# Kernel tuning notes

Measured on AMD Instinct MI355X. Metric: run time of the kernel, lower is better.

Reference implementation:

```python
import jax, jax.numpy as jnp
import numpy as np

NUM_HEADS = 8
C = 512


def setup_inputs() -> dict:
    key = jax.random.key(0)
    ks = jax.random.split(key, 8)
    B, D, H, W = 1, 16, 16, 16
    x = jax.random.normal(ks[0], (B, C, D, H, W), dtype=jnp.float32)
    s = 1.0 / np.sqrt(C)
    Wq = jax.random.normal(ks[1], (C, C), dtype=jnp.float32) * s
    Wk = jax.random.normal(ks[2], (C, C), dtype=jnp.float32) * s
    Wv = jax.random.normal(ks[3], (C, C), dtype=jnp.float32) * s
    bq = jax.random.normal(ks[4], (C,), dtype=jnp.float32) * 0.01
    bk = jax.random.normal(ks[5], (C,), dtype=jnp.float32) * 0.01
    bv = jax.random.normal(ks[6], (C,), dtype=jnp.float32) * 0.01
    # torch inits gamma to 0; use 0.5 so the attention branch contributes
    gamma = jnp.full((1,), 0.5, dtype=jnp.float32)
    return {"x": x, "Wq": Wq, "bq": bq, "Wk": Wk, "bk": bk, "Wv": Wv, "bv": bv, "gamma": gamma}


def _attn(x, Wq, bq, Wk, bk, Wv, bv, gamma):
    B, Cc, D, H, W = x.shape
    nh = NUM_HEADS
    hd = Cc // nh
    N = D * H * W

    def proj(Wm, bm):
        # 1x1x1 Conv3d == channel GEMM
        y = jnp.einsum('oc,bcdhw->bodhw', Wm, x) + bm[None, :, None, None, None]
        y = y.reshape(B, nh, hd, D, H, W)            # [B, nh, hd, D, H, W]
        y = jnp.moveaxis(y, 2, -1)                    # [B, nh, D, H, W, hd]
        return y.reshape(B * nh, N, hd)               # [B*nh, N, hd]

    q = proj(Wq, bq)
    k = proj(Wk, bk)
    v = proj(Wv, bv)

    # NOTE: original module has NO 1/sqrt(head_dim) scaling -- faithful.
    energy = jnp.einsum('bnd,bmd->bnm', q, k)         # [B*nh, N, N]
    attention = jax.nn.softmax(energy, axis=-1)
    out = jnp.einsum('bnm,bmd->bnd', attention, v)    # [B*nh, N, hd]

    # Faithful (buggy-in-original) reshape: [B, N, nh, hd] row-major into [B, C, D, H, W]
    out = out.reshape(B, nh, N, hd).transpose(0, 2, 1, 3).reshape(B, Cc, D, H, W)
    return gamma[0] * out + x


def reference(x, Wq, bq, Wk, bk, Wv, bv, gamma):
    return _attn(x, Wq, bq, Wk, bk, Wv, bv, gamma)
```

## Files before the change

### kernel.cpp

```cpp
#include <hip/hip_runtime.h>

typedef unsigned short u16;
typedef __attribute__((ext_vector_type(4))) float f32x4;
typedef __attribute__((ext_vector_type(8))) short s16x8;
typedef __attribute__((ext_vector_type(4))) unsigned short u16x4;
typedef __attribute__((ext_vector_type(8))) unsigned short u16x8;
typedef __attribute__((ext_vector_type(2))) unsigned int u32x2;

#define MFMA(a, b, c) __builtin_amdgcn_mfma_f32_16x16x32_bf16((a), (b), (c), 0, 0, 0)

#define XT_HI 0u
#define XT_LO 2097152u
#define W_HI  4194304u
#define W_LO  4980736u
#define Q_HI  5767168u
#define Q_LO  7864320u
#define K_HI  9961472u
#define K_LO  12058624u
#define V_HI  14155776u
#define V_LO  16252928u
#define WS_BYTES_U16 36700160u

__device__ __forceinline__ u16 f2bf(float f) {
  union { float f; unsigned u; } v; v.f = f;
  unsigned r = v.u + 0x7fffu + ((v.u >> 16) & 1u);
  return (u16)(r >> 16);
}
__device__ __forceinline__ float bf2f(u16 h) {
  union { unsigned u; float f; } v; v.u = ((unsigned)h) << 16;
  return v.f;
}
__device__ __forceinline__ unsigned pk2(float a, float b) {
  return (unsigned)f2bf(a) | ((unsigned)f2bf(b) << 16);
}
__device__ __forceinline__ void gload16(const void* g, void* l) {
  __builtin_amdgcn_global_load_lds(
      (const __attribute__((address_space(1))) void*)g,
      (__attribute__((address_space(3))) void*)l, 16, 0, 0);
}

__global__ __launch_bounds__(256) void prep_w(const float* __restrict__ wq,
                                              const float* __restrict__ wk,
                                              const float* __restrict__ wv,
                                              u16* __restrict__ ws) {
  unsigned t = blockIdx.x * 256u + threadIdx.x;
  unsigned idx = t * 4u;
  unsigned which = idx >> 18;
  unsigned rem = idx & 262143u;
  const float* src = (which == 0) ? wq : (which == 1) ? wk : wv;
  f32x4 v = *(const f32x4*)(src + rem);
  u16x4 h, l;
#pragma unroll
  for (int i = 0; i < 4; ++i) {
    u16 hb = f2bf(v[i]);
    h[i] = hb;
    l[i] = f2bf(v[i] - bf2f(hb));
  }
  *(u16x4*)(ws + W_HI + idx) = h;
  *(u16x4*)(ws + W_LO + idx) = l;
}

__global__ __launch_bounds__(256) void prep_xt(const float* __restrict__ x,
                                               u16* __restrict__ ws) {
  __shared__ float tile[64][65];
  unsigned t = threadIdx.x;
  unsigned n0 = blockIdx.x * 64u, c0 = blockIdx.y * 64u;
  unsigned cl = t >> 2, ns = (t & 3u) * 16u;
  const float* src = x + (c0 + cl) * 4096u + n0 + ns;
#pragma unroll
  for (int j = 0; j < 16; j += 4) {
    f32x4 v = *(const f32x4*)(src + j);
#pragma unroll
    for (int e = 0; e < 4; ++e) tile[cl][ns + j + e] = v[e];
  }
  __syncthreads();
  unsigned nl = t >> 2, cs = (t & 3u) * 16u;
  u16x8 vh0, vh1, vl0, vl1;
#pragma unroll
  for (int j = 0; j < 16; ++j) {
    float v = tile[cs + j][nl];
    u16 hb = f2bf(v);
    u16 lb = f2bf(v - bf2f(hb));
    if (j < 8) { vh0[j] = hb; vl0[j] = lb; }
    else       { vh1[j - 8] = hb; vl1[j - 8] = lb; }
  }
  unsigned off = (n0 + nl) * 512u + c0 + cs;
  *(u16x8*)(ws + XT_HI + off) = vh0;
  *(u16x8*)(ws + XT_HI + off + 8u) = vh1;
  *(u16x8*)(ws + XT_LO + off) = vl0;
  *(u16x8*)(ws + XT_LO + off + 8u) = vl1;
}

__global__ __launch_bounds__(256) void proj(const float* __restrict__ bq,
                                            const float* __restrict__ bk,
                                            const float* __restrict__ bv,
                                            u16* __restrict__ ws) {
  __shared__ u16 sm[24576];
  const unsigned t = threadIdx.x, w = t >> 6, lane = t & 63u;
  const unsigned g4 = lane >> 4, c = lane & 15u;
  const unsigned z = blockIdx.z;
  const unsigned m0 = blockIdx.y * 64u, n0 = blockIdx.x * 128u;
  const unsigned wo = w >> 1, wn = w & 1u;

  const u16* WHp = ws + W_HI + z * 262144u;
  const u16* WLp = ws + W_LO + z * 262144u;
  const u16* XH = ws + XT_HI;
  const u16* XL = ws + XT_LO;

  f32x4 acc[2][4];
#pragma unroll
  for (int a = 0; a < 2; ++a)
#pragma unroll
    for (int b = 0; b < 4; ++b) acc[a][b] = (f32x4){0.f, 0.f, 0.f, 0.f};

  const unsigned r_l = lane >> 3;
  const unsigned cl_ = lane & 7u;

  for (unsigned it = 0; it < 8; ++it) {
    unsigned k0 = it * 64u;
#pragma unroll
    for (unsigned j = 0; j < 12; ++j) {
      unsigned s = w * 12u + j;
      if (s < 8u) {
        unsigned r = 8u * s + r_l; unsigned cg = cl_ ^ (r & 7u);
        gload16(WHp + (m0 + r) * 512u + k0 + 8u * cg, sm + s * 512u);
      } else if (s < 16u) {
        unsigned sl = s - 8u; unsigned r = 8u * sl + r_l; unsigned cg = cl_ ^ (r & 7u);
        gload16(WLp + (m0 + r) * 512u + k0 + 8u * cg, sm + 4096u + sl * 512u);
      } else if (s < 32u) {
        unsigned sl = s - 16u; unsigned r = 8u * sl + r_l; unsigned cg = cl_ ^ (r & 7u);
        gload16(XH + (n0 + r) * 512u + k0 + 8u * cg, sm + 8192u + sl * 512u);
      } else {
        unsigned sl = s - 32u; unsigned r = 8u * sl + r_l; unsigned cg = cl_ ^ (r & 7u);
        gload16(XL + (n0 + r) * 512u + k0 + 8u * cg, sm + 16384u + sl * 512u);
      }
    }
    __syncthreads();

    s16x8 ah[2][2], al[2][2];
#pragma unroll
    for (int mr = 0; mr < 2; ++mr)
#pragma unroll
      for (int ks = 0; ks < 2; ++ks) {
        unsigned row = 32u * wo + 16u * mr + c;
        unsigned idx = row * 64u + (((g4 + 4u * ks) ^ (row & 7u)) * 8u);
        ah[mr][ks] = *(const s16x8*)(sm + idx);
        al[mr][ks] = *(const s16x8*)(sm + 4096u + idx);
      }
#pragma unroll
    for (int ks = 0; ks < 2; ++ks)
#pragma unroll
      for (int nr = 0; nr < 4; ++nr) {
        unsigned row = 64u * wn + 16u * nr + c;
        unsigned idx = row * 64u + (((g4 + 4u * ks) ^ (row & 7u)) * 8u);
        s16x8 bh = *(const s16x8*)(sm + 8192u + idx);
        s16x8 bl = *(const s16x8*)(sm + 16384u + idx);
#pragma unroll
        for (int mr = 0; mr < 2; ++mr) {
          acc[mr][nr] = MFMA(ah[mr][ks], bh, acc[mr][nr]);
          acc[mr][nr] = MFMA(ah[mr][ks], bl, acc[mr][nr]);
          acc[mr][nr] = MFMA(al[mr][ks], bh, acc[mr][nr]);
        }
      }
    __syncthreads();
  }

  const float* bias = (z == 0) ? bq : (z == 1) ? bk : bv;
  const unsigned obase = m0 + 32u * wo;
#pragma unroll
  for (int mr = 0; mr < 2; ++mr) {
    f32x4 b4 = *(const f32x4*)(bias + obase + 16u * mr + 4u * g4);
#pragma unroll
    for (int nr = 0; nr < 4; ++nr) {
      unsigned n = n0 + 64u * wn + 16u * nr + c;
      float v4[4];
#pragma unroll
      for (int i = 0; i < 4; ++i) v4[i] = acc[mr][nr][i] + b4[i];
      if (z < 2u) {
        unsigned d0 = 32u * wo + 16u * mr + 4u * g4;
        unsigned off = (blockIdx.y * 4096u + n) * 64u + d0;
        u16* dh = ws + (z ? K_HI : Q_HI) + off;
        u16* dl = ws + (z ? K_LO : Q_LO) + off;
        u16x4 h4, l4;
#pragma unroll
        for (int i = 0; i < 4; ++i) {
          u16 hb = f2bf(v4[i]);
          h4[i] = hb;
          l4[i] = f2bf(v4[i] - bf2f(hb));
        }
        *(u16x4*)dh = h4;
        *(u16x4*)dl = l4;
      } else {
#pragma unroll
        for (int i = 0; i < 4; ++i) {
          unsigned o = obase + 16u * mr + 4u * g4 + i;
          ws[V_HI + o * 4096u + n] = f2bf(v4[i]);
        }
      }
    }
  }
}

__global__ __launch_bounds__(256) void attn(const u16* __restrict__ ws,
                                            float* __restrict__ ows,
                                            float* __restrict__ lws) {
  extern __shared__ u16 sm[];
  const unsigned t = threadIdx.x, w = t >> 6, lane = t & 63u;
  const unsigned g4 = lane >> 4, c = lane & 15u;
  const unsigned h = blockIdx.y, sp = blockIdx.z;
  const unsigned q0 = blockIdx.x * 128u;

  const u16* QHp = ws + Q_HI; const u16* QLp = ws + Q_LO;
  const u16* KHp = ws + K_HI; const u16* KLp = ws + K_LO;
  const u16* VHp = ws + V_HI;

  s16x8 qh[2][2], ql[2][2];
#pragma unroll
  for (int mq = 0; mq < 2; ++mq)
#pragma unroll
    for (int ks = 0; ks < 2; ++ks) {
      unsigned q = q0 + 32u * w + 16u * mq + c;
      unsigned off = (h * 4096u + q) * 64u + 8u * g4 + 32u * ks;
      qh[mq][ks] = *(const s16x8*)(QHp + off);
      ql[mq][ks] = *(const s16x8*)(QLp + off);
    }

  f32x4 O[2][4];
#pragma unroll
  for (int a = 0; a < 2; ++a)
#pragma unroll
    for (int b = 0; b < 4; ++b) O[a][b] = (f32x4){0.f, 0.f, 0.f, 0.f};
  float lr[2] = {0.f, 0.f};

  const unsigned r_l = lane >> 3, cl_ = lane & 7u;
  u16* Pw = sm + 24576u + w * 2048u;

  auto stage = [&](unsigned b, unsigned ch) {
    unsigned n0 = sp * 2048u + ch * 64u;
#pragma unroll
    for (unsigned j = 0; j < 6u; ++j) {
      unsigned s = w * 6u + j;
      unsigned pl = s >> 3, sl = s & 7u;
      unsigned r = 8u * sl + r_l;
      unsigned cg = cl_ ^ (r & 7u);
      const u16* gsrc;
      if (pl == 0u)      gsrc = KHp + (h * 4096u + n0 + r) * 64u + 8u * cg;
      else if (pl == 1u) gsrc = KLp + (h * 4096u + n0 + r) * 64u + 8u * cg;
      else               gsrc = VHp + (h * 64u + r) * 4096u + n0 + 8u * cg;
      gload16(gsrc, sm + b * 12288u + pl * 4096u + sl * 512u);
    }
  };

  stage(0u, 0u);
  __syncthreads();

  unsigned cur = 0u;
  for (unsigned ch = 0; ch < 32u; ++ch) {
    if (ch < 31u) stage(cur ^ 1u, ch + 1u);
    const unsigned kb = cur * 12288u;

    f32x4 S[2][4];
#pragma unroll
    for (int a = 0; a < 2; ++a)
#pragma unroll
      for (int b = 0; b < 4; ++b) S[a][b] = (f32x4){0.f, 0.f, 0.f, 0.f};
#pragma unroll
    for (int ks = 0; ks < 2; ++ks)
#pragma unroll
      for (int nr = 0; nr < 4; ++nr) {
        unsigned row = 16u * nr + c;
        unsigned idx = kb + row * 64u + (((g4 + 4u * ks) ^ (row & 7u)) * 8u);
        s16x8 kh = *(const s16x8*)(sm + idx);
        s16x8 kl = *(const s16x8*)(sm + 4096u + idx);
#pragma unroll
        for (int mq = 0; mq < 2; ++mq) {
          S[mq][nr] = MFMA(kh, qh[mq][ks], S[mq][nr]);
          S[mq][nr] = MFMA(kl, qh[mq][ks], S[mq][nr]);
          S[mq][nr] = MFMA(kh, ql[mq][ks], S[mq][nr]);
        }
      }

#pragma unroll
    for (int mq = 0; mq < 2; ++mq) {
      unsigned q = 16u * mq + c;
      float ls = 0.f;
#pragma unroll
      for (int nr = 0; nr < 4; ++nr) {
        f32x4 s = S[mq][nr];
        float p0 = __expf(s[0] - 40.0f);
        float p1 = __expf(s[1] - 40.0f);
        float p2 = __expf(s[2] - 40.0f);
        float p3 = __expf(s[3] - 40.0f);
        ls += (p0 + p1) + (p2 + p3);
        u32x2 pv;
        pv[0] = pk2(p0, p1);
        pv[1] = pk2(p2, p3);
        unsigned off = q * 64u + (((2u * nr + (g4 >> 1)) ^ (c & 7u)) * 8u) + (g4 & 1u) * 4u;
        *(u32x2*)(Pw + off) = pv;
      }
      ls += __shfl_xor(ls, 16);
      ls += __shfl_xor(ls, 32);
      lr[mq] += ls;
    }

#pragma unroll
    for (int ks = 0; ks < 2; ++ks) {
      s16x8 pa[2];
#pragma unroll
      for (int mr = 0; mr < 2; ++mr)
        pa[mr] = *(const s16x8*)(Pw + (16u * mr + c) * 64u +
                                 (((g4 + 4u * ks) ^ (c & 7u)) * 8u));
#pragma unroll
      for (int nr = 0; nr < 4; ++nr) {
        unsigned row = 16u * nr + c;
        unsigned idx = kb + 8192u + row * 64u + (((g4 + 4u * ks) ^ (row & 7u)) * 8u);
        s16x8 vh = *(const s16x8*)(sm + idx);
#pragma unroll
        for (int mr = 0; mr < 2; ++mr)
          O[mr][nr] = MFMA(pa[mr], vh, O[mr][nr]);
      }
    }
    __syncthreads();
    cur ^= 1u;
  }

#pragma unroll
  for (int mr = 0; mr < 2; ++mr)
#pragma unroll
    for (int i = 0; i < 4; ++i) {
      unsigned n = q0 + 32u * w + 16u * mr + 4u * g4 + i;
      unsigned lwi = (sp * 8u + h) * 4096u + n;
#pragma unroll
      for (int nr = 0; nr < 4; ++nr)
        ows[lwi * 64u + 16u * nr + c] = O[mr][nr][i];
    }
  if (lane < 16u) {
#pragma unroll
    for (int mq = 0; mq < 2; ++mq)
      lws[(sp * 8u + h) * 4096u + q0 + 32u * w + 16u * mq + lane] = lr[mq];
  }
}

__global__ __launch_bounds__(256) void combine(const float* __restrict__ x,
                                               const float* __restrict__ gamma,
                                               const float* __restrict__ ows,
                                               const float* __restrict__ lws,
                                               float* __restrict__ out) {
  unsigned t = blockIdx.x * 256u + threadIdx.x;
  unsigned L = t * 4u;
  unsigned n = L >> 9, hd6 = L & 511u, h = hd6 >> 6, d = L & 63u;
  unsigned i0 = (h * 4096u + n) * 64u + d;
  unsigned i1 = ((8u + h) * 4096u + n) * 64u + d;
  f32x4 a = *(const f32x4*)(ows + i0);
  f32x4 b = *(const f32x4*)(ows + i1);
  float l = lws[h * 4096u + n] + lws[(8u + h) * 4096u + n];
  float gi = gamma[0] / l;
  f32x4 xv = *(const f32x4*)(x + L);
  f32x4 r = (a + b) * gi + xv;
  *(f32x4*)(out + L) = r;
}

extern "C" void kernel_launch(void* const* d_in, const int* in_sizes, int n_in,
                              void* d_out, int out_size, void* d_ws, size_t ws_size,
                              hipStream_t stream) {
  const float* x = (const float*)d_in[0];
  const float* wq = (const float*)d_in[1];
  const float* bq = (const float*)d_in[2];
  const float* wk = (const float*)d_in[3];
  const float* bk = (const float*)d_in[4];
  const float* wv = (const float*)d_in[5];
  const float* bv = (const float*)d_in[6];
  const float* gamma = (const float*)d_in[7];
  u16* ws = (u16*)d_ws;
  float* ows = (float*)((char*)d_ws + WS_BYTES_U16);
  float* lws = ows + 4194304u;
  float* out = (float*)d_out;

  prep_w<<<dim3(768), dim3(256), 0, stream>>>(wq, wk, wv, ws);
  prep_xt<<<dim3(64, 8), dim3(256), 0, stream>>>(x, ws);
  proj<<<dim3(32, 8, 3), dim3(256), 0, stream>>>(bq, bk, bv, ws);
  (void)hipFuncSetAttribute((const void*)attn,
                            hipFuncAttributeMaxDynamicSharedMemorySize, 65536);
  attn<<<dim3(32, 8, 2), dim3(256), 65536, stream>>>(ws, ows, lws);
  combine<<<dim3(2048), dim3(256), 0, stream>>>(x, gamma, ows, lws, out);
}
```

Measured before the change: 196.6 us.

## Drop K low-bf16 split and halve the attention query tile per block

The projection now stores K only as a single bf16 value and drops the low-residual half. The QK^T product therefore takes two MFMAs (kh·qh, kh·ql) instead of three, and each K/V stage only loads K-hi and V. The attention kernel also goes from 32 to 16 queries per wave (64 per block), doubling the grid and cutting dynamic LDS from 64KB to 40KB to allow more resident blocks. The cost is less K precision in unscaled logits that feed exp, and twice the global K/V traffic, since each block reuses a K/V tile over fewer queries.

```diff
diff --git a/kernel.cpp b/kernel.cpp
--- a/kernel.cpp
+++ b/kernel.cpp
@@ -176,11 +176,9 @@
       float v4[4];
 #pragma unroll
       for (int i = 0; i < 4; ++i) v4[i] = acc[mr][nr][i] + b4[i];
-      if (z < 2u) {
+      if (z == 0u) {
         unsigned d0 = 32u * wo + 16u * mr + 4u * g4;
         unsigned off = (blockIdx.y * 4096u + n) * 64u + d0;
-        u16* dh = ws + (z ? K_HI : Q_HI) + off;
-        u16* dl = ws + (z ? K_LO : Q_LO) + off;
         u16x4 h4, l4;
 #pragma unroll
         for (int i = 0; i < 4; ++i) {
@@ -188,8 +186,15 @@
           h4[i] = hb;
           l4[i] = f2bf(v4[i] - bf2f(hb));
         }
-        *(u16x4*)dh = h4;
-        *(u16x4*)dl = l4;
+        *(u16x4*)(ws + Q_HI + off) = h4;
+        *(u16x4*)(ws + Q_LO + off) = l4;
+      } else if (z == 1u) {
+        unsigned d0 = 32u * wo + 16u * mr + 4u * g4;
+        unsigned off = (blockIdx.y * 4096u + n) * 64u + d0;
+        u16x4 h4;
+#pragma unroll
+        for (int i = 0; i < 4; ++i) h4[i] = f2bf(v4[i]);
+        *(u16x4*)(ws + K_HI + off) = h4;
       } else {
 #pragma unroll
         for (int i = 0; i < 4; ++i) {
@@ -208,46 +213,41 @@
   const unsigned t = threadIdx.x, w = t >> 6, lane = t & 63u;
   const unsigned g4 = lane >> 4, c = lane & 15u;
   const unsigned h = blockIdx.y, sp = blockIdx.z;
-  const unsigned q0 = blockIdx.x * 128u;
+  const unsigned q0 = blockIdx.x * 64u;
 
   const u16* QHp = ws + Q_HI; const u16* QLp = ws + Q_LO;
-  const u16* KHp = ws + K_HI; const u16* KLp = ws + K_LO;
+  const u16* KHp = ws + K_HI;
   const u16* VHp = ws + V_HI;
 
-  s16x8 qh[2][2], ql[2][2];
-#pragma unroll
-  for (int mq = 0; mq < 2; ++mq)
-#pragma unroll
-    for (int ks = 0; ks < 2; ++ks) {
-      unsigned q = q0 + 32u * w + 16u * mq + c;
-      unsigned off = (h * 4096u + q) * 64u + 8u * g4 + 32u * ks;
-      qh[mq][ks] = *(const s16x8*)(QHp + off);
-      ql[mq][ks] = *(const s16x8*)(QLp + off);
-    }
-
-  f32x4 O[2][4];
-#pragma unroll
-  for (int a = 0; a < 2; ++a)
-#pragma unroll
-    for (int b = 0; b < 4; ++b) O[a][b] = (f32x4){0.f, 0.f, 0.f, 0.f};
-  float lr[2] = {0.f, 0.f};
+  s16x8 qh[2], ql[2];
+#pragma unroll
+  for (int ks = 0; ks < 2; ++ks) {
+    unsigned q = q0 + 16u * w + c;
+    unsigned off = (h * 4096u + q) * 64u + 8u * g4 + 32u * ks;
+    qh[ks] = *(const s16x8*)(QHp + off);
+    ql[ks] = *(const s16x8*)(QLp + off);
+  }
+
+  f32x4 O[4];
+#pragma unroll
+  for (int b = 0; b < 4; ++b) O[b] = (f32x4){0.f, 0.f, 0.f, 0.f};
+  float lr = 0.f;
 
   const unsigned r_l = lane >> 3, cl_ = lane & 7u;
-  u16* Pw = sm + 24576u + w * 2048u;
+  u16* Pw = sm + 16384u + w * 1024u;
 
   auto stage = [&](unsigned b, unsigned ch) {
     unsigned n0 = sp * 2048u + ch * 64u;
 #pragma unroll
-    for (unsigned j = 0; j < 6u; ++j) {
-      unsigned s = w * 6u + j;
+    for (unsigned j = 0; j < 4u; ++j) {
+      unsigned s = w * 4u + j;
       unsigned pl = s >> 3, sl = s & 7u;
       unsigned r = 8u * sl + r_l;
       unsigned cg = cl_ ^ (r & 7u);
       const u16* gsrc;
-      if (pl == 0u)      gsrc = KHp + (h * 4096u + n0 + r) * 64u + 8u * cg;
-      else if (pl == 1u) gsrc = KLp + (h * 4096u + n0 + r) * 64u + 8u * cg;
-      else               gsrc = VHp + (h * 64u + r) * 4096u + n0 + 8u * cg;
-      gload16(gsrc, sm + b * 12288u + pl * 4096u + sl * 512u);
+      if (pl == 0u) gsrc = KHp + (h * 4096u + n0 + r) * 64u + 8u * cg;
+      else          gsrc = VHp + (h * 64u + r) * 4096u + n0 + 8u * cg;
+      gload16(gsrc, sm + b * 8192u + pl * 4096u + sl * 512u);
     }
   };
 
@@ -257,13 +257,11 @@
   unsigned cur = 0u;
   for (unsigned ch = 0; ch < 32u; ++ch) {
     if (ch < 31u) stage(cur ^ 1u, ch + 1u);
-    const unsigned kb = cur * 12288u;
-
-    f32x4 S[2][4];
-#pragma unroll
-    for (int a = 0; a < 2; ++a)
-#pragma unroll
-      for (int b = 0; b < 4; ++b) S[a][b] = (f32x4){0.f, 0.f, 0.f, 0.f};
+    const unsigned kb = cur * 8192u;
+
+    f32x4 S[4];
+#pragma unroll
+    for (int b = 0; b < 4; ++b) S[b] = (f32x4){0.f, 0.f, 0.f, 0.f};
 #pragma unroll
     for (int ks = 0; ks < 2; ++ks)
 #pragma unroll
@@ -271,22 +269,15 @@
         unsigned row = 16u * nr + c;
         unsigned idx = kb + row * 64u + (((g4 + 4u * ks) ^ (row & 7u)) * 8u);
         s16x8 kh = *(const s16x8*)(sm + idx);
-        s16x8 kl = *(const s16x8*)(sm + 4096u + idx);
-#pragma unroll
-        for (int mq = 0; mq < 2; ++mq) {
-          S[mq][nr] = MFMA(kh, qh[mq][ks], S[mq][nr]);
-          S[mq][nr] = MFMA(kl, qh[mq][ks], S[mq][nr]);
-          S[mq][nr] = MFMA(kh, ql[mq][ks], S[mq][nr]);
-        }
-      }
-
-#pragma unroll
-    for (int mq = 0; mq < 2; ++mq) {
-      unsigned q = 16u * mq + c;
+        S[nr] = MFMA(kh, qh[ks], S[nr]);
+        S[nr] = MFMA(kh, ql[ks], S[nr]);
+      }
+
+    {
       float ls = 0.f;
 #pragma unroll
       for (int nr = 0; nr < 4; ++nr) {
-        f32x4 s = S[mq][nr];
+        f32x4 s = S[nr];
         float p0 = __expf(s[0] - 40.0f);
         float p1 = __expf(s[1] - 40.0f);
         float p2 = __expf(s[2] - 40.0f);
@@ -295,29 +286,23 @@
         u32x2 pv;
         pv[0] = pk2(p0, p1);
         pv[1] = pk2(p2, p3);
-        unsigned off = q * 64u + (((2u * nr + (g4 >> 1)) ^ (c & 7u)) * 8u) + (g4 & 1u) * 4u;
+        unsigned off = c * 64u + (((2u * nr + (g4 >> 1)) ^ (c & 7u)) * 8u) + (g4 & 1u) * 4u;
         *(u32x2*)(Pw + off) = pv;
       }
       ls += __shfl_xor(ls, 16);
       ls += __shfl_xor(ls, 32);
-      lr[mq] += ls;
+      lr += ls;
     }
 
 #pragma unroll
     for (int ks = 0; ks < 2; ++ks) {
-      s16x8 pa[2];
-#pragma unroll
-      for (int mr = 0; mr < 2; ++mr)
-        pa[mr] = *(const s16x8*)(Pw + (16u * mr + c) * 64u +
-                                 (((g4 + 4u * ks) ^ (c & 7u)) * 8u));
+      s16x8 pa = *(const s16x8*)(Pw + c * 64u + (((g4 + 4u * ks) ^ (c & 7u)) * 8u));
 #pragma unroll
       for (int nr = 0; nr < 4; ++nr) {
         unsigned row = 16u * nr + c;
-        unsigned idx = kb + 8192u + row * 64u + (((g4 + 4u * ks) ^ (row & 7u)) * 8u);
+        unsigned idx = kb + 4096u + row * 64u + (((g4 + 4u * ks) ^ (row & 7u)) * 8u);
         s16x8 vh = *(const s16x8*)(sm + idx);
-#pragma unroll
-        for (int mr = 0; mr < 2; ++mr)
-          O[mr][nr] = MFMA(pa[mr], vh, O[mr][nr]);
+        O[nr] = MFMA(pa, vh, O[nr]);
       }
     }
     __syncthreads();
@@ -325,20 +310,15 @@
   }
 
 #pragma unroll
-  for (int mr = 0; mr < 2; ++mr)
-#pragma unroll
-    for (int i = 0; i < 4; ++i) {
-      unsigned n = q0 + 32u * w + 16u * mr + 4u * g4 + i;
-      unsigned lwi = (sp * 8u + h) * 4096u + n;
-#pragma unroll
-      for (int nr = 0; nr < 4; ++nr)
-        ows[lwi * 64u + 16u * nr + c] = O[mr][nr][i];
-    }
-  if (lane < 16u) {
-#pragma unroll
-    for (int mq = 0; mq < 2; ++mq)
-      lws[(sp * 8u + h) * 4096u + q0 + 32u * w + 16u * mq + lane] = lr[mq];
-  }
+  for (int i = 0; i < 4; ++i) {
+    unsigned n = q0 + 16u * w + 4u * g4 + i;
+    unsigned lwi = (sp * 8u + h) * 4096u + n;
+#pragma unroll
+    for (int nr = 0; nr < 4; ++nr)
+      ows[lwi * 64u + 16u * nr + c] = O[nr][i];
+  }
+  if (lane < 16u)
+    lws[(sp * 8u + h) * 4096u + q0 + 16u * w + lane] = lr;
 }
 
 __global__ __launch_bounds__(256) void combine(const float* __restrict__ x,
@@ -380,7 +360,7 @@
   prep_xt<<<dim3(64, 8), dim3(256), 0, stream>>>(x, ws);
   proj<<<dim3(32, 8, 3), dim3(256), 0, stream>>>(bq, bk, bv, ws);
   (void)hipFuncSetAttribute((const void*)attn,
-                            hipFuncAttributeMaxDynamicSharedMemorySize, 65536);
-  attn<<<dim3(32, 8, 2), dim3(256), 65536, stream>>>(ws, ows, lws);
+                            hipFuncAttributeMaxDynamicSharedMemorySize, 40960);
+  attn<<<dim3(64, 8, 2), dim3(256), 40960, stream>>>(ws, ows, lws);
   combine<<<dim3(2048), dim3(256), 0, stream>>>(x, gamma, ows, lws, out);
 }
```

Result: faster. 188.1 us (-4.4%).
